# Performance work log

Hardware: AMD Instinct MI355X
Metric: run time of the kernel (lower is better)

The kernel has to match this reference:

```python
import jax, jax.numpy as jnp
import numpy as np

K_SPRING = 1.0
B_DAMP = 0.1
M_MASS = 1.0
DT = 0.01
T_STEPS = 2048
BATCH_N = 4096


def _make_A():
    A = jnp.array([[-B_DAMP / M_MASS, 0.0, -K_SPRING / M_MASS, 0.0],
                   [0.0, -B_DAMP / M_MASS, 0.0, -K_SPRING / M_MASS],
                   [1.0, 0.0, 0.0, 0.0],
                   [0.0, 1.0, 0.0, 0.0]], dtype=jnp.float32)
    return A * DT + jnp.eye(4, dtype=jnp.float32)


def setup_inputs() -> dict:
    key = jax.random.key(0)
    k1, k2 = jax.random.split(key)
    z_and_L_hat = jax.random.normal(k1, (T_STEPS, BATCH_N, 5), dtype=jnp.float32)
    mu0 = jax.random.normal(k2, (BATCH_N, 4), dtype=jnp.float32)
    return {"z_and_L_hat": z_and_L_hat, "mu0": mu0}


def reference(z_and_L_hat, mu0):
    A = _make_A()                                    # [4,4]
    C = jnp.array([[0.0, 0.0, 1.0, 0.0],
                   [0.0, 0.0, 0.0, 1.0]], dtype=jnp.float32)  # [2,4]
    I4 = jnp.eye(4, dtype=jnp.float32)
    # Bw @ Q @ Bw.T with Q = I2, Bw = [[1,0],[0,1],[0,0],[0,0]] -> diag(1,1,0,0)
    BwQBw = jnp.diag(jnp.array([1.0, 1.0, 0.0, 0.0], dtype=jnp.float32))
    N = mu0.shape[0]
    Sig0 = jnp.broadcast_to(jnp.eye(4, dtype=jnp.float32), (N, 4, 4))

    def step(carry, zl):
        mu, Sig = carry                              # [N,4], [N,4,4]
        z = zl[:, 0:2]                               # [N,2]
        Lh = zl[:, 2:5]                              # [N,3]
        # predict
        mu_pred = mu @ A.T                           # [N,4]
        Sig_pred = jnp.einsum('ij,njk,lk->nil', A, Sig, A) + BwQBw  # [N,4,4]
        # R = L L^T with L = [[exp(l0),0],[l1,exp(l2)]]
        l00 = jnp.exp(Lh[:, 0])
        l10 = Lh[:, 1]
        l11 = jnp.exp(Lh[:, 2])
        R00 = l00 * l00
        R01 = l00 * l10
        R11 = l10 * l10 + l11 * l11
        R = jnp.stack([jnp.stack([R00, R01], -1),
                       jnp.stack([R01, R11], -1)], -2)             # [N,2,2]
        # S = C Sig_pred C^T + R ; C selects state rows/cols 2:4
        S = Sig_pred[:, 2:4, 2:4] + R                # [N,2,2]
        # closed-form 2x2 inverse
        det = S[:, 0, 0] * S[:, 1, 1] - S[:, 0, 1] * S[:, 1, 0]
        Sinv = jnp.stack([jnp.stack([S[:, 1, 1], -S[:, 0, 1]], -1),
                          jnp.stack([-S[:, 1, 0], S[:, 0, 0]], -1)], -2) / det[:, None, None]
        K = Sig_pred[:, :, 2:4] @ Sinv               # [N,4,2] == Sig_pred C^T Sinv
        innov = z - mu_pred[:, 2:4]                  # z - C mu_pred
        mu_out = mu_pred + jnp.einsum('nij,nj->ni', K, innov)      # [N,4]
        Sig_out = (I4 - K @ C) @ Sig_pred            # [N,4,4]
        y = mu_out[:, 2:4]                           # C mu_out
        return (mu_out, Sig_out), y

    _, y_hats = jax.lax.scan(step, (mu0, Sig0), z_and_L_hat)
    return y_hats                                    # [T,N,2]
```

## Files before the change

### kernel.cpp

```cpp
#include <hip/hip_runtime.h>


#define TS 8

__global__ __launch_bounds__(64, 1)
void kalman_lds(const float* __restrict__ zl,
                const float* __restrict__ mu0,
                float* __restrict__ out,
                int N, int T)
{
    __shared__ float lds[2][5][TS][64];

    const int lane = threadIdx.x;
    const int n    = blockIdx.x * 64 + lane;

    const float a  = 0.999f;
    const float cA = -0.01f;
    const float dA = 0.01f;

    float4 m4 = reinterpret_cast<const float4*>(mu0)[n];
    float m0 = m4.x, m1 = m4.y, m2 = m4.z, m3 = m4.w;

    float P00=1.f, P01=0.f, P02=0.f, P03=0.f;
    float P11=1.f, P12=0.f, P13=0.f;
    float P22=1.f, P23=0.f, P33=1.f;

    const long step5N  = (long)N * 5;
    const long strideY = (long)N * 2;
    const float* zlane = zl + (long)n * 5;
    float* outp        = out + (long)n * 2;

    #pragma unroll
    for (int s = 0; s < TS; ++s) {
        const float* g = zlane + (long)s * step5N;
        #pragma unroll
        for (int j = 0; j < 5; ++j) {
            __builtin_amdgcn_global_load_lds(
                (const __attribute__((address_space(1))) unsigned int*)(g + j),
                (__attribute__((address_space(3))) unsigned int*)&lds[0][j][s][0],
                4, 0, 0);
        }
    }
    asm volatile("s_waitcnt vmcnt(0)" ::: "memory");

    const int NT = T / TS;
    for (int tile = 0; tile < NT; ++tile) {
        const int b = tile & 1;

        asm volatile("s_waitcnt vmcnt(8)" ::: "memory");

        float r[TS * 5];
        #pragma unroll
        for (int s = 0; s < TS; ++s) {
            #pragma unroll
            for (int j = 0; j < 5; ++j)
                r[s * 5 + j] = lds[b][j][s][lane];
        }

        {
            const int nt = (tile + 1 < NT) ? (tile + 1) : 0;
            const float* gb = zlane + (long)nt * TS * step5N;
            #pragma unroll
            for (int s = 0; s < TS; ++s) {
                const float* g = gb + (long)s * step5N;
                #pragma unroll
                for (int j = 0; j < 5; ++j) {
                    __builtin_amdgcn_global_load_lds(
                        (const __attribute__((address_space(1))) unsigned int*)(g + j),
                        (__attribute__((address_space(3))) unsigned int*)&lds[b ^ 1][j][s][0],
                        4, 0, 0);
                }
            }
        }

        float* yp = outp + (long)(tile * TS) * strideY;

        #pragma unroll
        for (int s = 0; s < TS; ++s) {
            const float z0 = r[s*5+0], z1 = r[s*5+1];
            const float L0 = r[s*5+2], L1 = r[s*5+3], L2 = r[s*5+4];

            float mp0 = a * m0 + cA * m2;
            float mp1 = a * m1 + cA * m3;
            float mp2 = dA * m0 + m2;
            float mp3 = dA * m1 + m3;

            float M00 = a * P00 + cA * P02;
            float M01 = a * P01 + cA * P12;
            float M02 = a * P02 + cA * P22;
            float M03 = a * P03 + cA * P23;
            float M10 = a * P01 + cA * P03;
            float M11 = a * P11 + cA * P13;
            float M12 = a * P12 + cA * P23;
            float M13 = a * P13 + cA * P33;
            float M20 = dA * P00 + P02;
            float M21 = dA * P01 + P12;
            float M22 = dA * P02 + P22;
            float M23 = dA * P03 + P23;
            float M30 = dA * P01 + P03;
            float M31 = dA * P11 + P13;
            float M33 = dA * P13 + P33;

            float Q00 = a * M00 + cA * M02 + 1.0f;
            float Q01 = a * M01 + cA * M03;
            float Q02 = dA * M00 + M02;
            float Q03 = dA * M01 + M03;
            float Q11 = a * M11 + cA * M13 + 1.0f;
            float Q12 = dA * M10 + M12;
            float Q13 = dA * M11 + M13;
            float Q22 = dA * M20 + M22;
            float Q23 = dA * M21 + M23;
            float Q33 = dA * M31 + M33;

            float l00 = __expf(L0);
            float l10 = L1;
            float l11 = __expf(L2);
            float R00 = l00 * l00;
            float R01 = l00 * l10;
            float R11 = l10 * l10 + l11 * l11;

            float S00 = Q22 + R00;
            float S01 = Q23 + R01;
            float S11 = Q33 + R11;
            float det = S00 * S11 - S01 * S01;
            float inv = __builtin_amdgcn_rcpf(det);
            float iS00 = S11 * inv;
            float iS01 = -S01 * inv;
            float iS11 = S00 * inv;

            float K00 = Q02 * iS00 + Q03 * iS01;
            float K01 = Q02 * iS01 + Q03 * iS11;
            float K10 = Q12 * iS00 + Q13 * iS01;
            float K11 = Q12 * iS01 + Q13 * iS11;
            float K20 = Q22 * iS00 + Q23 * iS01;
            float K21 = Q22 * iS01 + Q23 * iS11;
            float K30 = Q23 * iS00 + Q33 * iS01;
            float K31 = Q23 * iS01 + Q33 * iS11;

            float in0 = z0 - mp2;
            float in1 = z1 - mp3;
            m0 = mp0 + K00 * in0 + K01 * in1;
            m1 = mp1 + K10 * in0 + K11 * in1;
            m2 = mp2 + K20 * in0 + K21 * in1;
            m3 = mp3 + K30 * in0 + K31 * in1;

            P00 = Q00 - K00 * Q02 - K01 * Q03;
            P01 = Q01 - K00 * Q12 - K01 * Q13;
            P02 = Q02 - K00 * Q22 - K01 * Q23;
            P03 = Q03 - K00 * Q23 - K01 * Q33;
            P11 = Q11 - K10 * Q12 - K11 * Q13;
            P12 = Q12 - K10 * Q22 - K11 * Q23;
            P13 = Q13 - K10 * Q23 - K11 * Q33;
            P22 = Q22 - K20 * Q22 - K21 * Q23;
            P23 = Q23 - K20 * Q23 - K21 * Q33;
            P33 = Q33 - K30 * Q23 - K31 * Q33;

            reinterpret_cast<float2*>(yp)[0] = make_float2(m2, m3);
            yp += strideY;
        }
    }
}

extern "C" void kernel_launch(void* const* d_in, const int* in_sizes, int n_in,
                              void* d_out, int out_size, void* d_ws, size_t ws_size,
                              hipStream_t stream) {
    const float* zl  = (const float*)d_in[0];
    const float* mu0 = (const float*)d_in[1];
    float* out = (float*)d_out;

    int N = in_sizes[1] / 4;
    int T = in_sizes[0] / (N * 5);

    int block = 64;
    int grid = N / block;
    kalman_lds<<<grid, block, 0, stream>>>(zl, mu0, out, N, T);
}
```

Measured before the change: 704.3 us.

## Split each Kalman filter across two lanes with shuffles for cross terms

Each batch element is now handled by a lane pair, one lane per spatial axis. Each lane keeps a 3-entry own-axis covariance block and a 4-entry cross block, and exchanges cross terms and innovations via xor shuffles. The grid doubles so more waves and compute units run the serial recurrence concurrently, and per-lane arithmetic shrinks. The cost is added cross-lane shuffle latency on the sequential dependency chain and a changed LDS staging layout.

New measurement: 716.0 us. No clear change (+1.7%).

```diff
diff --git a/kernel.cpp b/kernel.cpp
--- a/kernel.cpp
+++ b/kernel.cpp
@@ -4,159 +4,140 @@
 #define TS 8
 
 __global__ __launch_bounds__(64, 1)
-void kalman_lds(const float* __restrict__ zl,
-                const float* __restrict__ mu0,
-                float* __restrict__ out,
-                int N, int T)
+void kalman_pair(const float* __restrict__ zl,
+                 const float* __restrict__ mu0,
+                 float* __restrict__ out,
+                 int N, int T)
 {
-    __shared__ float lds[2][5][TS][64];
+    __shared__ float lds[2][5][TS][32];
 
-    const int lane = threadIdx.x;
-    const int n    = blockIdx.x * 64 + lane;
+    const int l   = threadIdx.x;
+    const int p   = l >> 1;
+    const int isy = l & 1;
+    const int B   = blockIdx.x;
+    const int n   = B * 32 + p;
 
-    const float a  = 0.999f;
-    const float cA = -0.01f;
-    const float dA = 0.01f;
+    const float a = 0.999f;
+    const float c = -0.01f;
+    const float d = 0.01f;
 
-    float4 m4 = reinterpret_cast<const float4*>(mu0)[n];
-    float m0 = m4.x, m1 = m4.y, m2 = m4.z, m3 = m4.w;
+    float mv = mu0[n * 4 + isy];
+    float mp = mu0[n * 4 + 2 + isy];
+    float s0 = 1.f, s1 = 0.f, s2 = 1.f;
+    float w0 = 0.f, w1 = 0.f, w2 = 0.f, w3 = 0.f;
 
-    float P00=1.f, P01=0.f, P02=0.f, P03=0.f;
-    float P11=1.f, P12=0.f, P13=0.f;
-    float P22=1.f, P23=0.f, P33=1.f;
-
-    const long step5N  = (long)N * 5;
-    const long strideY = (long)N * 2;
-    const float* zlane = zl + (long)n * 5;
-    float* outp        = out + (long)n * 2;
-
-    #pragma unroll
-    for (int s = 0; s < TS; ++s) {
-        const float* g = zlane + (long)s * step5N;
+    auto stage = [&](int buf, int tb) {
+        const int s  = 2 * 0 + 0; (void)s;
         #pragma unroll
         for (int j = 0; j < 5; ++j) {
-            __builtin_amdgcn_global_load_lds(
-                (const __attribute__((address_space(1))) unsigned int*)(g + j),
-                (__attribute__((address_space(3))) unsigned int*)&lds[0][j][s][0],
-                4, 0, 0);
+            #pragma unroll
+            for (int q = 0; q < 4; ++q) {
+                const int ss = 2 * q + (l >> 5);
+                const int e  = l & 31;
+                const float* g = zl + ((size_t)(tb + ss) * N + B * 32 + e) * 5 + j;
+                __builtin_amdgcn_global_load_lds(
+                    (const __attribute__((address_space(1))) unsigned int*)g,
+                    (__attribute__((address_space(3))) unsigned int*)&lds[buf][j][2 * q][0],
+                    4, 0, 0);
+            }
         }
-    }
+    };
+
+    const float* Lb0 = &lds[0][0][0][0];
+    const float* Lb1 = &lds[1][0][0][0];
+    const int zoff = (isy ? 1 : 0) * (TS * 32) + p;
+    const int ooff = (isy ? 4 : 2) * (TS * 32) + p;
+    const int moff = 3 * (TS * 32) + p;
+
+    stage(0, 0);
     asm volatile("s_waitcnt vmcnt(0)" ::: "memory");
 
     const int NT = T / TS;
     for (int tile = 0; tile < NT; ++tile) {
         const int b = tile & 1;
+        const float* Lb = b ? Lb1 : Lb0;
 
         asm volatile("s_waitcnt vmcnt(8)" ::: "memory");
 
-        float r[TS * 5];
+        float rz[TS], ro[TS], rm[TS];
         #pragma unroll
         for (int s = 0; s < TS; ++s) {
-            #pragma unroll
-            for (int j = 0; j < 5; ++j)
-                r[s * 5 + j] = lds[b][j][s][lane];
+            rz[s] = Lb[zoff + s * 32];
+            ro[s] = Lb[ooff + s * 32];
+            rm[s] = Lb[moff + s * 32];
         }
 
         {
             const int nt = (tile + 1 < NT) ? (tile + 1) : 0;
-            const float* gb = zlane + (long)nt * TS * step5N;
-            #pragma unroll
-            for (int s = 0; s < TS; ++s) {
-                const float* g = gb + (long)s * step5N;
-                #pragma unroll
-                for (int j = 0; j < 5; ++j) {
-                    __builtin_amdgcn_global_load_lds(
-                        (const __attribute__((address_space(1))) unsigned int*)(g + j),
-                        (__attribute__((address_space(3))) unsigned int*)&lds[b ^ 1][j][s][0],
-                        4, 0, 0);
-                }
-            }
+            stage(b ^ 1, nt * TS);
         }
 
-        float* yp = outp + (long)(tile * TS) * strideY;
+        float* yp = out + (size_t)(tile * TS) * 2 * N + (size_t)B * 64 + l;
 
         #pragma unroll
         for (int s = 0; s < TS; ++s) {
-            const float z0 = r[s*5+0], z1 = r[s*5+1];
-            const float L0 = r[s*5+2], L1 = r[s*5+3], L2 = r[s*5+4];
+            const float z_own = rz[s], Lown = ro[s], L1v = rm[s];
 
-            float mp0 = a * m0 + cA * m2;
-            float mp1 = a * m1 + cA * m3;
-            float mp2 = dA * m0 + m2;
-            float mp3 = dA * m1 + m3;
+            float mpv = a * mv + c * mp;
+            float mpp = d * mv + mp;
 
-            float M00 = a * P00 + cA * P02;
-            float M01 = a * P01 + cA * P12;
-            float M02 = a * P02 + cA * P22;
-            float M03 = a * P03 + cA * P23;
-            float M10 = a * P01 + cA * P03;
-            float M11 = a * P11 + cA * P13;
-            float M12 = a * P12 + cA * P23;
-            float M13 = a * P13 + cA * P33;
-            float M20 = dA * P00 + P02;
-            float M21 = dA * P01 + P12;
-            float M22 = dA * P02 + P22;
-            float M23 = dA * P03 + P23;
-            float M30 = dA * P01 + P03;
-            float M31 = dA * P11 + P13;
-            float M33 = dA * P13 + P33;
+            float M0 = a * s0 + c * s1, M1 = a * s1 + c * s2;
+            float M2 = d * s0 + s1,     M3 = d * s1 + s2;
+            float s0p = a * M0 + (c * M1 + 1.0f);
+            float s1p = d * M0 + M1;
+            float s2p = d * M2 + M3;
 
-            float Q00 = a * M00 + cA * M02 + 1.0f;
-            float Q01 = a * M01 + cA * M03;
-            float Q02 = dA * M00 + M02;
-            float Q03 = dA * M01 + M03;
-            float Q11 = a * M11 + cA * M13 + 1.0f;
-            float Q12 = dA * M10 + M12;
-            float Q13 = dA * M11 + M13;
-            float Q22 = dA * M20 + M22;
-            float Q23 = dA * M21 + M23;
-            float Q33 = dA * M31 + M33;
+            float t0 = a * w0 + c * w2, t1 = a * w1 + c * w3;
+            float t2 = d * w0 + w2,     t3 = d * w1 + w3;
+            float w0p = a * t0 + c * t1;
+            float w1p = d * t0 + t1;
+            float w2p = a * t2 + c * t3;
+            float w3p = d * t2 + t3;
 
-            float l00 = __expf(L0);
-            float l10 = L1;
-            float l11 = __expf(L2);
-            float R00 = l00 * l00;
-            float R01 = l00 * l10;
-            float R11 = l10 * l10 + l11 * l11;
+            float sendA = isy ? s1p : w2p;
+            float recvA = __shfl_xor(sendA, 1);
+            float sendB = isy ? s2p : w3p;
+            float recvB = __shfl_xor(sendB, 1);
 
-            float S00 = Q22 + R00;
-            float S01 = Q23 + R01;
-            float S11 = Q33 + R11;
-            float det = S00 * S11 - S01 * S01;
+            float le = __expf(Lown);
+            float tt = isy ? L1v : 0.0f;
+            float Rd = le * le + tt * tt;
+
+            float S_own = s2p + Rd;
+            float S_oth = __shfl_xor(S_own, 1);
+            float S01x  = le * L1v + w3p;
+            float S01r  = __shfl_xor(S01x, 1);
+            float S01   = isy ? S01r : S01x;
+
+            float det = S_own * S_oth - S01 * S01;
             float inv = __builtin_amdgcn_rcpf(det);
-            float iS00 = S11 * inv;
-            float iS01 = -S01 * inv;
-            float iS11 = S00 * inv;
+            float iSa =  S_oth * inv;
+            float iSb = -S01 * inv;
+            float iSc =  S_own * inv;
 
-            float K00 = Q02 * iS00 + Q03 * iS01;
-            float K01 = Q02 * iS01 + Q03 * iS11;
-            float K10 = Q12 * iS00 + Q13 * iS01;
-            float K11 = Q12 * iS01 + Q13 * iS11;
-            float K20 = Q22 * iS00 + Q23 * iS01;
-            float K21 = Q22 * iS01 + Q23 * iS11;
-            float K30 = Q23 * iS00 + Q33 * iS01;
-            float K31 = Q23 * iS01 + Q33 * iS11;
+            float bv = isy ? recvA : w1p;
+            float bp = isy ? recvB : w3p;
+            float Kv0 = s1p * iSa + bv * iSb;
+            float Kv1 = s1p * iSb + bv * iSc;
+            float Kp0 = s2p * iSa + bp * iSb;
+            float Kp1 = s2p * iSb + bp * iSc;
 
-            float in0 = z0 - mp2;
-            float in1 = z1 - mp3;
-            m0 = mp0 + K00 * in0 + K01 * in1;
-            m1 = mp1 + K10 * in0 + K11 * in1;
-            m2 = mp2 + K20 * in0 + K21 * in1;
-            m3 = mp3 + K30 * in0 + K31 * in1;
+            float in_own = z_own - mpp;
+            float in_oth = __shfl_xor(in_own, 1);
+            mv = mpv + Kv0 * in_own + Kv1 * in_oth;
+            mp = mpp + Kp0 * in_own + Kp1 * in_oth;
 
-            P00 = Q00 - K00 * Q02 - K01 * Q03;
-            P01 = Q01 - K00 * Q12 - K01 * Q13;
-            P02 = Q02 - K00 * Q22 - K01 * Q23;
-            P03 = Q03 - K00 * Q23 - K01 * Q33;
-            P11 = Q11 - K10 * Q12 - K11 * Q13;
-            P12 = Q12 - K10 * Q22 - K11 * Q23;
-            P13 = Q13 - K10 * Q23 - K11 * Q33;
-            P22 = Q22 - K20 * Q22 - K21 * Q23;
-            P23 = Q23 - K20 * Q23 - K21 * Q33;
-            P33 = Q33 - K30 * Q23 - K31 * Q33;
+            s0 = s0p - Kv0 * s1p - Kv1 * bv;
+            s1 = s1p - Kv0 * s2p - Kv1 * bp;
+            s2 = s2p - Kp0 * s2p - Kp1 * bp;
 
-            reinterpret_cast<float2*>(yp)[0] = make_float2(m2, m3);
-            yp += strideY;
+            w0 = w0p - Kv0 * w2p - Kv1 * recvA;
+            w1 = w1p - Kv0 * w3p - Kv1 * recvB;
+            w2 = w2p - Kp0 * w2p - Kp1 * recvA;
+            w3 = w3p - Kp0 * w3p - Kp1 * recvB;
+
+            *yp = mp;
+            yp += (size_t)2 * N;
         }
     }
 }
@@ -172,6 +153,6 @@
     int T = in_sizes[0] / (N * 5);
 
     int block = 64;
-    int grid = N / block;
-    kalman_lds<<<grid, block, 0, stream>>>(zl, mu0, out, N, T);
+    int grid  = N / 32;
+    kalman_pair<<<grid, block, 0, stream>>>(zl, mu0, out, N, T);
 }
```
